# Kernel tuning notes

Measured on AMD Instinct MI355X. Metric: run time of the kernel, lower is better.

## Reference

```python
import jax, jax.numpy as jnp
import numpy as np

N_NODES = 100_000
N_EDGES_RAND = 800_000
N_GRAPHS = 2048
IN_FEATS = 74        # CanonicalAtomFeaturizer size
HEADS = 4            # dgllife GAT default num_heads
OUT_FEATS = 32       # dgllife GAT default hidden_feats=[32,32]
PRED_DIM = 128
NEG_SLOPE = 0.2      # dgllife default alpha


def setup_inputs() -> dict:
    key = jax.random.key(0)
    ks = jax.random.split(key, 16)
    feats = jax.random.normal(ks[0], (N_NODES, IN_FEATS), jnp.float32)
    src_r = jax.random.randint(ks[1], (N_EDGES_RAND,), 0, N_NODES, dtype=jnp.int32)
    dst_r = jax.random.randint(ks[2], (N_EDGES_RAND,), 0, N_NODES, dtype=jnp.int32)
    loops = jnp.arange(N_NODES, dtype=jnp.int32)  # self-loops -> no zero in-degree
    src = jnp.concatenate([src_r, loops])
    dst = jnp.concatenate([dst_r, loops])
    # sorted, every graph non-empty, ~49 nodes per molecule
    graph_ids = ((jnp.arange(N_NODES, dtype=jnp.int64) * N_GRAPHS) // N_NODES).astype(jnp.int32)

    def lin(k, i, o):
        return (jax.random.normal(k, (i, o), jnp.float32) / np.sqrt(i)).astype(jnp.float32)

    HF = HEADS * OUT_FEATS
    return {
        'feats': feats, 'src': src, 'dst': dst, 'graph_ids': graph_ids,
        'fc1_w': lin(ks[3], IN_FEATS, HF),
        'attn_l1': jax.random.normal(ks[4], (HEADS, OUT_FEATS), jnp.float32) * 0.1,
        'attn_r1': jax.random.normal(ks[5], (HEADS, OUT_FEATS), jnp.float32) * 0.1,
        'res1_w': lin(ks[6], IN_FEATS, HF),   # residual proj (in != heads*out)
        'bias1': jnp.zeros((HF,), jnp.float32),
        'fc2_w': lin(ks[7], HF, HF),
        'attn_l2': jax.random.normal(ks[8], (HEADS, OUT_FEATS), jnp.float32) * 0.1,
        'attn_r2': jax.random.normal(ks[9], (HEADS, OUT_FEATS), jnp.float32) * 0.1,
        'bias2': jnp.zeros((HF,), jnp.float32),
        'ww': lin(ks[10], OUT_FEATS, 1),
        'wb': jnp.zeros((1,), jnp.float32),
        'tw': lin(ks[11], 2 * OUT_FEATS, PRED_DIM),
        'tb': jnp.zeros((PRED_DIM,), jnp.float32),
    }


def _gat_conv(h, src, dst, fc_w, attn_l, attn_r, bias, res):
    # h: (N, Din) -> (N, H, F). Faithful to dgl.nn.GATConv (bias=True, residual=True).
    N = h.shape[0]
    feat = (h @ fc_w).reshape(N, HEADS, OUT_FEATS)          # (N,H,F)
    el = jnp.sum(feat * attn_l, axis=-1)                    # (N,H)
    er = jnp.sum(feat * attn_r, axis=-1)                    # (N,H)
    e = jax.nn.leaky_relu(el[src] + er[dst], NEG_SLOPE)     # (E,H)
    # edge softmax over incoming edges of each dst node (numerically stable)
    emax = jax.ops.segment_max(e, dst, num_segments=N)      # (N,H)
    ee = jnp.exp(e - emax[dst])
    denom = jax.ops.segment_sum(ee, dst, num_segments=N)    # (N,H)
    a = ee / denom[dst]                                     # (E,H)
    rst = jax.ops.segment_sum(a[:, :, None] * feat[src], dst, num_segments=N)  # (N,H,F)
    return rst + res + bias.reshape(1, HEADS, OUT_FEATS)


def reference(feats, src, dst, graph_ids, fc1_w, attn_l1, attn_r1, res1_w, bias1,
              fc2_w, attn_l2, attn_r2, bias2, ww, wb, tw, tb):
    N = feats.shape[0]
    # Layer 1: residual needs projection (74 != 128); agg 'flatten' + ELU
    res1 = (feats @ res1_w).reshape(N, HEADS, OUT_FEATS)
    h1 = _gat_conv(feats, src, dst, fc1_w, attn_l1, attn_r1, bias1, res1)
    h1 = jax.nn.elu(h1.reshape(N, HEADS * OUT_FEATS))
    # Layer 2: identity residual (128 == heads*out); agg 'mean', no activation
    res2 = h1.reshape(N, HEADS, OUT_FEATS)
    h2 = _gat_conv(h1, src, dst, fc2_w, attn_l2, attn_r2, bias2, res2)
    node_feats = jnp.mean(h2, axis=1)                       # (N, 32)
    # WeightedSumAndMax readout
    w = jax.nn.sigmoid(node_feats @ ww + wb)                # (N,1)
    h_sum = jax.ops.segment_sum(w * node_feats, graph_ids, num_segments=N_GRAPHS)
    h_max = jax.ops.segment_max(node_feats, graph_ids, num_segments=N_GRAPHS)
    g = jnp.concatenate([h_sum, h_max], axis=-1)            # (B, 64)
    return g @ tw + tb                                      # (B, PRED_DIM)
```

## Files before the change

kernel.cpp:

```cpp
#include <hip/hip_runtime.h>
#include <hip/hip_bf16.h>


#define HEADS 4
#define OUTF 32
#define HF 128
#define IN_FEATS 74
#define PRED_DIM 128
#define NEG_SLOPE 0.2f
#define NEG_INF_ENC 0x007fffffu
#define LOG2E 1.4426950408889634f
#define KP1 48
#define KP2 64
#define LSTR1 52
#define LSTR2 68

typedef __hip_bfloat16 bf16;
typedef __hip_bfloat162 bf16x2;
typedef __attribute__((ext_vector_type(8))) short bf16x8v;
typedef __attribute__((ext_vector_type(4))) float f32x4v;
typedef __attribute__((ext_vector_type(2))) float f32x2v;

__device__ __forceinline__ unsigned enc_f(float f) {
  unsigned u = __float_as_uint(f);
  return (u & 0x80000000u) ? ~u : (u | 0x80000000u);
}
__device__ __forceinline__ float dec_f(unsigned k) {
  return (k & 0x80000000u) ? __uint_as_float(k & 0x7fffffffu)
                           : __uint_as_float(~k);
}
__device__ __forceinline__ unsigned pack_bf16(float a, float b) {
  bf16x2 h = __float22bfloat162_rn(make_float2(a, b));
  return *(unsigned*)&h;
}
__device__ __forceinline__ float2 unpack_bf16(unsigned u) {
  bf16x2 h = *(bf16x2*)&u;
  return __bfloat1622float2(h);
}
__device__ __forceinline__ float lrelu(float v) {
  return fmaxf(v, NEG_SLOPE * v);
}

__global__ __launch_bounds__(256) void hist_prep(
    const int* __restrict__ dst, int* __restrict__ deg,
    int* __restrict__ rank, float* __restrict__ hsum,
    unsigned* __restrict__ hmax, int E, int g32,
    const float* __restrict__ W1, const float* __restrict__ W2,
    const float* __restrict__ W3, unsigned* __restrict__ WT1,
    unsigned* __restrict__ WT2, unsigned* __restrict__ WT3) {
  int t = blockIdx.x * 256 + threadIdx.x;
  if (t < g32) {
    hsum[t] = 0.f;
    hmax[t] = NEG_INF_ENC;
  }
  if (t < 128 * KP1) {
    int c = t / KP1, kp = t % KP1;
    int k = kp * 2;
    float a1 = (k < IN_FEATS) ? W1[k * HF + c] : 0.f;
    float b1 = (k + 1 < IN_FEATS) ? W1[(k + 1) * HF + c] : 0.f;
    float a2 = (k < IN_FEATS) ? W2[k * HF + c] : 0.f;
    float b2 = (k + 1 < IN_FEATS) ? W2[(k + 1) * HF + c] : 0.f;
    WT1[t] = pack_bf16(a1, b1);
    WT2[t] = pack_bf16(a2, b2);
  } else if (t - 128 * KP1 < 128 * KP2) {
    int u = t - 128 * KP1;
    int c = u / KP2, kp = u % KP2;
    int k = kp * 2;
    WT3[u] = pack_bf16(W3[k * HF + c], W3[(k + 1) * HF + c]);
  }
  if (t < E) rank[t] = atomicAdd(&deg[dst[t]], 1);
}

__global__ __launch_bounds__(256) void scan12_kernel(
    const int* __restrict__ deg, int* __restrict__ row_ptr,
    int* __restrict__ bsum, int* __restrict__ bpre,
    int* __restrict__ ticket, int N, int E) {
  const int base = blockIdx.x * 2048;
  const int tbase = base + threadIdx.x * 8;
  int vals[8];
  int tsum = 0;
#pragma unroll
  for (int i = 0; i < 8; ++i) {
    int idx = tbase + i;
    vals[i] = (idx < N) ? deg[idx] : 0;
    tsum += vals[i];
  }
  const int lane = threadIdx.x & 63, wv = threadIdx.x >> 6;
  int incl = tsum;
#pragma unroll
  for (int off = 1; off < 64; off <<= 1) {
    int nv = __shfl_up(incl, off);
    if (lane >= off) incl += nv;
  }
  __shared__ int wsum[4];
  __shared__ int isLast;
  if (lane == 63) wsum[wv] = incl;
  __syncthreads();
  int woff = 0;
  for (int w = 0; w < wv; ++w) woff += wsum[w];
  int run = woff + incl - tsum;
#pragma unroll
  for (int i = 0; i < 8; ++i) {
    int idx = tbase + i;
    if (idx < N) row_ptr[idx] = run;
    run += vals[i];
  }
  if (threadIdx.x == 255) {
    bsum[blockIdx.x] = woff + incl;
    __threadfence();
    int t = atomicAdd(ticket, 1);
    isLast = (t == (int)gridDim.x - 1);
  }
  __syncthreads();
  if (isLast) {
    if (threadIdx.x < 64) {
      __threadfence();
      const int NB = gridDim.x;
      int running = 0;
      for (int c = 0; c < NB; c += 64) {
        int v = (c + lane < NB) ? bsum[c + lane] : 0;
        int incl2 = v;
#pragma unroll
        for (int off = 1; off < 64; off <<= 1) {
          int nv = __shfl_up(incl2, off);
          if (lane >= off) incl2 += nv;
        }
        if (c + lane < NB) bpre[c + lane] = running + incl2 - v;
        running += __shfl(incl2, 63);
      }
    }
    __syncthreads();
    if (threadIdx.x == 0) row_ptr[N] = E - bpre[N >> 11];
  }
}


template <int K>
__device__ __forceinline__ bf16x8v load_a_f32(const float* __restrict__ X,
                                              int row, int N, int ks, int q) {
  unsigned v[4] = {0u, 0u, 0u, 0u};
  if (row < N) {
    const float* base = X + (size_t)row * K;
    int k = ks * 32 + q * 8;
#pragma unroll
    for (int j = 0; j < 4; ++j) {
      int kk = k + j * 2;
      if (kk + 1 < K) {
        float2 f = *(const float2*)&base[kk];
        v[j] = pack_bf16(f.x, f.y);
      } else if (kk < K) {
        v[j] = pack_bf16(base[kk], 0.f);
      }
    }
  }
  union { unsigned u[4]; bf16x8v v8; } r;
  r.u[0] = v[0]; r.u[1] = v[1]; r.u[2] = v[2]; r.u[3] = v[3];
  return r.v8;
}

template <int KP, int LSTR, int THREADS>
__device__ __forceinline__ void stage_w(const unsigned* __restrict__ WT,
                                        unsigned* wl, int tid) {
#pragma unroll
  for (int u = tid; u < 128 * (KP / 4); u += THREADS) {
    int row = u / (KP / 4), c4 = u % (KP / 4);
    uint4 v = *(const uint4*)&WT[row * KP + c4 * 4];
    *(uint4*)&wl[row * LSTR + c4 * 4] = v;
  }
}

__device__ __forceinline__ void scores_epilogue_sw(
    const f32x4v* acc, const float* __restrict__ attn_l,
    const float* __restrict__ attn_r, float* __restrict__ el,
    float* __restrict__ er, int node, int q, int lane, int N) {
  float pl[4], pr[4];
#pragma unroll
  for (int h = 0; h < 4; ++h) {
    float sl = 0.f, sr = 0.f;
#pragma unroll
    for (int r = 0; r < 4; ++r) {
      float c0 = acc[2 * h][r], c1 = acc[2 * h + 1][r];
      sl = fmaf(c0, attn_l[h * 32 + q * 4 + r], sl);
      sl = fmaf(c1, attn_l[h * 32 + 16 + q * 4 + r], sl);
      sr = fmaf(c0, attn_r[h * 32 + q * 4 + r], sr);
      sr = fmaf(c1, attn_r[h * 32 + 16 + q * 4 + r], sr);
    }
    sl += __shfl_xor(sl, 16);
    sl += __shfl_xor(sl, 32);
    sr += __shfl_xor(sr, 16);
    sr += __shfl_xor(sr, 32);
    pl[h] = sl * LOG2E;
    pr[h] = sr * LOG2E;
  }
  if (lane < 16 && node < N) {
    *(float4*)&el[(size_t)node * 4] = make_float4(pl[0], pl[1], pl[2], pl[3]);
    *(float4*)&er[(size_t)node * 4] = make_float4(pr[0], pr[1], pr[2], pr[3]);
  }
}

__device__ __forceinline__ void store_ct(const f32x4v* acc,
                                         bf16* __restrict__ out, int node,
                                         int q, int N) {
  if (node < N) {
#pragma unroll
    for (int t = 0; t < 8; ++t) {
      unsigned lo = pack_bf16(acc[t][0], acc[t][1]);
      unsigned hi = pack_bf16(acc[t][2], acc[t][3]);
      *(uint2*)&out[(size_t)node * HF + t * 16 + q * 4] = make_uint2(lo, hi);
    }
  }
}

__global__ __launch_bounds__(512) void scat_mfma1(
    const int* __restrict__ src, const int* __restrict__ dst,
    const int* __restrict__ row_ptr, const int* __restrict__ bpre,
    const int* __restrict__ rank, int* __restrict__ ssorted, int E, int gblk,
    const float* __restrict__ X, const unsigned* __restrict__ WT1,
    const unsigned* __restrict__ WT2, const float* __restrict__ attn_l,
    const float* __restrict__ attn_r, bf16* __restrict__ outA,
    bf16* __restrict__ outB, float* __restrict__ el, float* __restrict__ er,
    int N) {
  __shared__ __align__(16) unsigned wlds[2][128 * LSTR1];
  if ((int)blockIdx.x >= gblk) {
    int e = ((int)blockIdx.x - gblk) * 512 + threadIdx.x;
    if (e >= E) return;
    if (e < 16) ssorted[E + e] = 0;
    int d = dst[e];
    ssorted[row_ptr[d] + bpre[d >> 11] + rank[e]] = src[e];
    return;
  }
  const int tid = threadIdx.x;
  stage_w<KP1, LSTR1, 512>(WT1, &wlds[0][0], tid);
  stage_w<KP1, LSTR1, 512>(WT2, &wlds[1][0], tid);
  __syncthreads();

  const int w = tid >> 6;
  const int lane = tid & 63;
  const int cc = lane & 15;
  const int q = lane >> 4;
  const int n0 = blockIdx.x * 128;
  const int node = n0 + w * 16 + cc;

  f32x4v acc1[8], acc2[8];
#pragma unroll
  for (int t = 0; t < 8; ++t) {
    acc1[t] = f32x4v{0.f, 0.f, 0.f, 0.f};
    acc2[t] = f32x4v{0.f, 0.f, 0.f, 0.f};
  }

  constexpr int KSTEPS = (IN_FEATS + 31) / 32;
#pragma unroll
  for (int ks = 0; ks < KSTEPS; ++ks) {
    bf16x8v a = load_a_f32<IN_FEATS>(X, node, N, ks, q);
#pragma unroll
    for (int t = 0; t < 8; ++t) {
      bf16x8v b1 =
          *(const bf16x8v*)&wlds[0][(t * 16 + cc) * LSTR1 + ks * 16 + q * 4];
      bf16x8v b2 =
          *(const bf16x8v*)&wlds[1][(t * 16 + cc) * LSTR1 + ks * 16 + q * 4];
      acc1[t] = __builtin_amdgcn_mfma_f32_16x16x32_bf16(b1, a, acc1[t], 0, 0, 0);
      acc2[t] = __builtin_amdgcn_mfma_f32_16x16x32_bf16(b2, a, acc2[t], 0, 0, 0);
    }
  }
  store_ct(acc1, outA, node, q, N);
  store_ct(acc2, outB, node, q, N);
  scores_epilogue_sw(acc1, attn_l, attn_r, el, er, node, q, lane, N);
}

template <int K, int KP, int LSTR>
__global__ __launch_bounds__(512) void mfma_gemm(
    const bf16* __restrict__ X, const unsigned* __restrict__ WT,
    const float* __restrict__ attn_l, const float* __restrict__ attn_r,
    bf16* __restrict__ out, float* __restrict__ el, float* __restrict__ er,
    int N) {
  __shared__ __align__(16) unsigned wlds[128 * LSTR];
  const int tid = threadIdx.x;
  stage_w<KP, LSTR, 512>(WT, wlds, tid);
  __syncthreads();

  const int w = tid >> 6;
  const int lane = tid & 63;
  const int cc = lane & 15;
  const int q = lane >> 4;
  const int n0 = blockIdx.x * 128;
  const int node = n0 + w * 16 + cc;

  f32x4v acc[8];
#pragma unroll
  for (int t = 0; t < 8; ++t) acc[t] = f32x4v{0.f, 0.f, 0.f, 0.f};

  constexpr int KSTEPS = (K + 31) / 32;
#pragma unroll
  for (int ks = 0; ks < KSTEPS; ++ks) {
    bf16x8v a = *(const bf16x8v*)&X[(size_t)node * K + ks * 32 + q * 8];
#pragma unroll
    for (int t = 0; t < 8; ++t) {
      bf16x8v b =
          *(const bf16x8v*)&wlds[(t * 16 + cc) * LSTR + ks * 16 + q * 4];
      acc[t] = __builtin_amdgcn_mfma_f32_16x16x32_bf16(b, a, acc[t], 0, 0, 0);
    }
  }
  store_ct(acc, out, node, q, N);
  scores_epilogue_sw(acc, attn_l, attn_r, el, er, node, q, lane, N);
}


#define E8_LOAD(i, e_)                                                      \
  const int s##i = __builtin_amdgcn_readfirstlane(ssorted[e_]);             \
  const float xl##i = el[(unsigned)s##i * HEADS + h];                       \
  const unsigned fu##i = *(const unsigned*)&feat[(unsigned)s##i * HF + c2];
#define E8_CALC(i)                                                          \
  {                                                                         \
    float xx = __builtin_amdgcn_exp2f(lrelu(xl##i + ern));                  \
    f32x2v ff;                                                              \
    ff.x = __uint_as_float(fu##i << 16);                                    \
    ff.y = __uint_as_float(fu##i & 0xffff0000u);                            \
    ssum += xx;                                                             \
    axy = __builtin_elementwise_fma(f32x2v{xx, xx}, ff, axy);               \
  }
#define E8_CALC_PRED(i, e_)                                                 \
  {                                                                         \
    float xx = __builtin_amdgcn_exp2f(lrelu(xl##i + ern));                  \
    xx = ((e_) + i < re) ? xx : 0.f;                                        \
    f32x2v ff;                                                              \
    ff.x = __uint_as_float(fu##i << 16);                                    \
    ff.y = __uint_as_float(fu##i & 0xffff0000u);                            \
    ssum += xx;                                                             \
    axy = __builtin_elementwise_fma(f32x2v{xx, xx}, ff, axy);               \
  }

#define AGG_LOOP                                                            \
  f32x2v axy = {0.f, 0.f};                                                  \
  float ssum = 0.f;                                                         \
  const int dg = re - rb;                                                   \
  if (dg <= 8) {                                                            \
    E8_LOAD(0, rb) E8_LOAD(1, rb + 1) E8_LOAD(2, rb + 2)                    \
    E8_LOAD(3, rb + 3) E8_LOAD(4, rb + 4) E8_LOAD(5, rb + 5)                \
    E8_LOAD(6, rb + 6) E8_LOAD(7, rb + 7)                                   \
    E8_CALC_PRED(0, rb) E8_CALC_PRED(1, rb) E8_CALC_PRED(2, rb)             \
    E8_CALC_PRED(3, rb) E8_CALC_PRED(4, rb) E8_CALC_PRED(5, rb)             \
    E8_CALC_PRED(6, rb) E8_CALC_PRED(7, rb)                                 \
  } else if (dg <= 16) {                                                    \
    E8_LOAD(0, rb) E8_LOAD(1, rb + 1) E8_LOAD(2, rb + 2)                    \
    E8_LOAD(3, rb + 3) E8_LOAD(4, rb + 4) E8_LOAD(5, rb + 5)                \
    E8_LOAD(6, rb + 6) E8_LOAD(7, rb + 7)                                   \
    E8_LOAD(8, rb + 8) E8_LOAD(9, rb + 9) E8_LOAD(10, rb + 10)              \
    E8_LOAD(11, rb + 11) E8_LOAD(12, rb + 12) E8_LOAD(13, rb + 13)          \
    E8_LOAD(14, rb + 14) E8_LOAD(15, rb + 15)                               \
    E8_CALC(0) E8_CALC(1) E8_CALC(2) E8_CALC(3)                             \
    E8_CALC(4) E8_CALC(5) E8_CALC(6) E8_CALC(7)                             \
    E8_CALC_PRED(8, rb) E8_CALC_PRED(9, rb) E8_CALC_PRED(10, rb)            \
    E8_CALC_PRED(11, rb) E8_CALC_PRED(12, rb) E8_CALC_PRED(13, rb)          \
    E8_CALC_PRED(14, rb) E8_CALC_PRED(15, rb)                               \
  } else {                                                                  \
    int e = rb;                                                             \
    for (; e + 8 <= re; e += 8) {                                           \
      E8_LOAD(0, e) E8_LOAD(1, e + 1) E8_LOAD(2, e + 2) E8_LOAD(3, e + 3)   \
      E8_LOAD(4, e + 4) E8_LOAD(5, e + 5) E8_LOAD(6, e + 6)                 \
      E8_LOAD(7, e + 7)                                                     \
      E8_CALC(0) E8_CALC(1) E8_CALC(2) E8_CALC(3)                           \
      E8_CALC(4) E8_CALC(5) E8_CALC(6) E8_CALC(7)                           \
    }                                                                       \
    if (e < re) {                                                           \
      E8_LOAD(0, e) E8_LOAD(1, e + 1) E8_LOAD(2, e + 2) E8_LOAD(3, e + 3)   \
      E8_LOAD(4, e + 4) E8_LOAD(5, e + 5) E8_LOAD(6, e + 6)                 \
      E8_LOAD(7, e + 7)                                                     \
      E8_CALC_PRED(0, e) E8_CALC_PRED(1, e) E8_CALC_PRED(2, e)              \
      E8_CALC_PRED(3, e) E8_CALC_PRED(4, e) E8_CALC_PRED(5, e)              \
      E8_CALC_PRED(6, e) E8_CALC_PRED(7, e)                                 \
    }                                                                       \
  }                                                                         \
  float ax = axy.x, ay = axy.y;

__global__ __launch_bounds__(256) void agg1_fused(
    const int* __restrict__ row_ptr, const int* __restrict__ bpre,
    const int* __restrict__ ssorted, const float* __restrict__ el,
    const float* __restrict__ er, const bf16* __restrict__ feat,
    const bf16* __restrict__ res, bf16* __restrict__ H,
    const float* __restrict__ bias, int N) {
  int n = blockIdx.x * 4 + (threadIdx.x >> 6);
  if (n >= N) return;
  const int lane = threadIdx.x & 63;
  const int c2 = lane * 2, h = lane >> 4;
  const int rb =
      __builtin_amdgcn_readfirstlane(row_ptr[n] + bpre[n >> 11]);
  const int re =
      __builtin_amdgcn_readfirstlane(row_ptr[n + 1] + bpre[(n + 1) >> 11]);
  const float ern = er[(unsigned)n * HEADS + h];

  AGG_LOOP

  float inv = 1.f / ssum;
  float2 r = unpack_bf16(*(const unsigned*)&res[(unsigned)n * HF + c2]);
  float2 bi = *(const float2*)&bias[c2];
  float vx = fmaf(ax, inv, r.x + bi.x);
  float vy = fmaf(ay, inv, r.y + bi.y);
  vx = (vx > 0.f) ? vx : expm1f(vx);
  vy = (vy > 0.f) ? vy : expm1f(vy);
  *(unsigned*)&H[(unsigned)n * HF + c2] = pack_bf16(vx, vy);
}

__global__ __launch_bounds__(256) void agg2_fused(
    const int* __restrict__ row_ptr, const int* __restrict__ bpre,
    const int* __restrict__ ssorted, const float* __restrict__ el,
    const float* __restrict__ er, const bf16* __restrict__ feat,
    const bf16* __restrict__ h1, const float* __restrict__ bias,
    const float* __restrict__ ww, const float* __restrict__ wb,
    const int* __restrict__ gids, float* __restrict__ hsum,
    unsigned* __restrict__ hmax, int N) {
  int n = blockIdx.x * 4 + (threadIdx.x >> 6);
  if (n >= N) return;
  const int lane = threadIdx.x & 63;
  const int c2 = lane * 2, h = lane >> 4;
  const int rb =
      __builtin_amdgcn_readfirstlane(row_ptr[n] + bpre[n >> 11]);
  const int re =
      __builtin_amdgcn_readfirstlane(row_ptr[n + 1] + bpre[(n + 1) >> 11]);
  const float ern = er[(unsigned)n * HEADS + h];

  AGG_LOOP

  float inv = 1.f / ssum;
  float2 r = unpack_bf16(*(const unsigned*)&h1[(unsigned)n * HF + c2]);
  float2 bi = *(const float2*)&bias[c2];
  ax = fmaf(ax, inv, r.x + bi.x);
  ay = fmaf(ay, inv, r.y + bi.y);
#pragma unroll
  for (int off = 16; off < 64; off <<= 1) {
    ax += __shfl_xor(ax, off);
    ay += __shfl_xor(ay, off);
  }
  ax *= 0.25f;
  ay *= 0.25f;
  int c = c2 & 31;
  float d = fmaf(ax, ww[c], ay * ww[c + 1]);
#pragma unroll
  for (int off = 1; off < 16; off <<= 1) d += __shfl_xor(d, off);
  float wv = 1.f / (1.f + __expf(-(d + wb[0])));
  if (lane < 16) {
    int g = gids[n];
    atomicAdd(&hsum[g * OUTF + c], wv * ax);
    atomicAdd(&hsum[g * OUTF + c + 1], wv * ay);
    atomicMax(&hmax[g * OUTF + c], enc_f(ax));
    atomicMax(&hmax[g * OUTF + c + 1], enc_f(ay));
  }
}

__global__ __launch_bounds__(256) void final_gemm_kernel(
    const float* __restrict__ hsum, const unsigned* __restrict__ hmax,
    const float* __restrict__ tw, const float* __restrict__ tb,
    float* __restrict__ out, int G) {
  __shared__ float tws[64 * PRED_DIM];
  for (int i = threadIdx.x; i < 64 * PRED_DIM; i += 256) tws[i] = tw[i];
  __syncthreads();
  int g = blockIdx.x * 2 + (threadIdx.x >> 7);
  int p = threadIdx.x & 127;
  if (g >= G) return;
  float acc = tb[p];
#pragma unroll
  for (int k = 0; k < OUTF; ++k)
    acc = fmaf(hsum[g * OUTF + k], tws[k * PRED_DIM + p], acc);
#pragma unroll
  for (int k = 0; k < OUTF; ++k)
    acc = fmaf(dec_f(hmax[g * OUTF + k]), tws[(OUTF + k) * PRED_DIM + p], acc);
  out[(size_t)g * PRED_DIM + p] = acc;
}

static inline int cdiv(long long a, int b) { return (int)((a + b - 1) / b); }

extern "C" void kernel_launch(void* const* d_in, const int* in_sizes, int n_in,
                              void* d_out, int out_size, void* d_ws,
                              size_t ws_size, hipStream_t stream) {
  const float* feats   = (const float*)d_in[0];
  const int*   src     = (const int*)d_in[1];
  const int*   dst     = (const int*)d_in[2];
  const int*   gids    = (const int*)d_in[3];
  const float* fc1_w   = (const float*)d_in[4];
  const float* attn_l1 = (const float*)d_in[5];
  const float* attn_r1 = (const float*)d_in[6];
  const float* res1_w  = (const float*)d_in[7];
  const float* bias1   = (const float*)d_in[8];
  const float* fc2_w   = (const float*)d_in[9];
  const float* attn_l2 = (const float*)d_in[10];
  const float* attn_r2 = (const float*)d_in[11];
  const float* bias2   = (const float*)d_in[12];
  const float* ww      = (const float*)d_in[13];
  const float* wb      = (const float*)d_in[14];
  const float* tw      = (const float*)d_in[15];
  const float* tb      = (const float*)d_in[16];
  float* out = (float*)d_out;

  const int N = in_sizes[0] / IN_FEATS;
  const int E = in_sizes[1];
  const int G = out_size / PRED_DIM;
  const int NB = cdiv(N, 2048);

  bf16* A = (bf16*)d_ws;
  bf16* B = A + (size_t)N * HF;
  bf16* H = B + (size_t)N * HF;
  float* el = (float*)(H + (size_t)N * HF);
  float* er = el + (size_t)N * HEADS;
  float* hsum = er + (size_t)N * HEADS;
  unsigned* hmax = (unsigned*)(hsum + (size_t)G * OUTF);
  int* deg     = (int*)(hmax + (size_t)G * OUTF);
  int* ticket  = deg + N;
  int* row_ptr = deg + N + 1;
  int* ssorted = row_ptr + (N + 1);
  int* rank    = ssorted + E + 16;
  int* bsum    = rank + E;
  int* bpre    = bsum + NB;
  unsigned* WT1 = (unsigned*)(((uintptr_t)(bpre + NB) + 15) &
                              ~(uintptr_t)15);
  unsigned* WT2 = WT1 + 128 * KP1;
  unsigned* WT3 = WT2 + 128 * KP1;

  const int gblk = cdiv(N, 128);
  const int nwblk = cdiv(N, 4);
  const int SB = cdiv(E, 256);
  const int SB512 = cdiv(E, 512);

  hipMemsetAsync(deg, 0, (size_t)(N + 1) * sizeof(int), stream);
  hist_prep<<<SB, 256, 0, stream>>>(dst, deg, rank, hsum, hmax, E, G * OUTF,
                                    fc1_w, res1_w, fc2_w, WT1, WT2, WT3);
  scan12_kernel<<<NB, 256, 0, stream>>>(deg, row_ptr, bsum, bpre, ticket, N,
                                        E);

  scat_mfma1<<<gblk + SB512, 512, 0, stream>>>(
      src, dst, row_ptr, bpre, rank, ssorted, E, gblk, feats, WT1, WT2,
      attn_l1, attn_r1, A, B, el, er, N);
  agg1_fused<<<nwblk, 256, 0, stream>>>(row_ptr, bpre, ssorted, el, er, A, B,
                                        H, bias1, N);

  mfma_gemm<HF, KP2, LSTR2><<<gblk, 512, 0, stream>>>(
      H, WT3, attn_l2, attn_r2, A, el, er, N);
  agg2_fused<<<nwblk, 256, 0, stream>>>(row_ptr, bpre, ssorted, el, er, A, H,
                                        bias2, ww, wb, gids, hsum, hmax, N);

  final_gemm_kernel<<<cdiv(G, 2), 256, 0, stream>>>(hsum, hmax, tw, tb, out, G);
}
```

Measured before the change: 315.0 us.

## Overlap second-half layer-1 aggregation with first-half layer-2 GEMM in one launch

```diff
diff --git a/kernel.cpp b/kernel.cpp
--- a/kernel.cpp
+++ b/kernel.cpp
@@ -209,6 +209,35 @@
       *(uint2*)&out[(size_t)node * HF + t * 16 + q * 4] = make_uint2(lo, hi);
     }
   }
+}
+
+__device__ __forceinline__ void gemm2_body(
+    const bf16* __restrict__ X, const unsigned* wlds,
+    const float* __restrict__ attn_l, const float* __restrict__ attn_r,
+    bf16* __restrict__ out, float* __restrict__ el2,
+    float* __restrict__ er2, int n0, int tid, int N) {
+  const int lane = tid & 63;
+  const int cc = lane & 15;
+  const int q = lane >> 4;
+  const int w = tid >> 6;
+  const int node = n0 + w * 16 + cc;
+
+  f32x4v acc[8];
+#pragma unroll
+  for (int t = 0; t < 8; ++t) acc[t] = f32x4v{0.f, 0.f, 0.f, 0.f};
+
+#pragma unroll
+  for (int ks = 0; ks < 4; ++ks) {
+    bf16x8v a = *(const bf16x8v*)&X[(size_t)node * HF + ks * 32 + q * 8];
+#pragma unroll
+    for (int t = 0; t < 8; ++t) {
+      bf16x8v b =
+          *(const bf16x8v*)&wlds[(t * 16 + cc) * LSTR2 + ks * 16 + q * 4];
+      acc[t] = __builtin_amdgcn_mfma_f32_16x16x32_bf16(b, a, acc[t], 0, 0, 0);
+    }
+  }
+  store_ct(acc, out, node, q, N);
+  scores_epilogue_sw(acc, attn_l, attn_r, el2, er2, node, q, lane, N);
 }
 
 __global__ __launch_bounds__(512) void scat_mfma1(
@@ -267,43 +296,17 @@
   scores_epilogue_sw(acc1, attn_l, attn_r, el, er, node, q, lane, N);
 }
 
-template <int K, int KP, int LSTR>
-__global__ __launch_bounds__(512) void mfma_gemm(
+__global__ __launch_bounds__(512) void mfma_gemm2(
     const bf16* __restrict__ X, const unsigned* __restrict__ WT,
     const float* __restrict__ attn_l, const float* __restrict__ attn_r,
-    bf16* __restrict__ out, float* __restrict__ el, float* __restrict__ er,
-    int N) {
-  __shared__ __align__(16) unsigned wlds[128 * LSTR];
-  const int tid = threadIdx.x;
-  stage_w<KP, LSTR, 512>(WT, wlds, tid);
+    bf16* __restrict__ out, float* __restrict__ el2, float* __restrict__ er2,
+    int t0, int N) {
+  __shared__ __align__(16) unsigned wlds[128 * LSTR2];
+  stage_w<KP2, LSTR2, 512>(WT, wlds, threadIdx.x);
   __syncthreads();
-
-  const int w = tid >> 6;
-  const int lane = tid & 63;
-  const int cc = lane & 15;
-  const int q = lane >> 4;
-  const int n0 = blockIdx.x * 128;
-  const int node = n0 + w * 16 + cc;
-
-  f32x4v acc[8];
-#pragma unroll
-  for (int t = 0; t < 8; ++t) acc[t] = f32x4v{0.f, 0.f, 0.f, 0.f};
-
-  constexpr int KSTEPS = (K + 31) / 32;
-#pragma unroll
-  for (int ks = 0; ks < KSTEPS; ++ks) {
-    bf16x8v a = *(const bf16x8v*)&X[(size_t)node * K + ks * 32 + q * 8];
-#pragma unroll
-    for (int t = 0; t < 8; ++t) {
-      bf16x8v b =
-          *(const bf16x8v*)&wlds[(t * 16 + cc) * LSTR + ks * 16 + q * 4];
-      acc[t] = __builtin_amdgcn_mfma_f32_16x16x32_bf16(b, a, acc[t], 0, 0, 0);
-    }
-  }
-  store_ct(acc, out, node, q, N);
-  scores_epilogue_sw(acc, attn_l, attn_r, el, er, node, q, lane, N);
-}
-
+  gemm2_body(X, wlds, attn_l, attn_r, out, el2, er2,
+             (t0 + (int)blockIdx.x) * 128, threadIdx.x, N);
+}
 
 #define E8_LOAD(i, e_)                                                      \
   const int s##i = __builtin_amdgcn_readfirstlane(ssorted[e_]);             \
@@ -372,15 +375,12 @@
   }                                                                         \
   float ax = axy.x, ay = axy.y;
 
-__global__ __launch_bounds__(256) void agg1_fused(
-    const int* __restrict__ row_ptr, const int* __restrict__ bpre,
-    const int* __restrict__ ssorted, const float* __restrict__ el,
-    const float* __restrict__ er, const bf16* __restrict__ feat,
-    const bf16* __restrict__ res, bf16* __restrict__ H,
-    const float* __restrict__ bias, int N) {
-  int n = blockIdx.x * 4 + (threadIdx.x >> 6);
-  if (n >= N) return;
-  const int lane = threadIdx.x & 63;
+__device__ __forceinline__ void agg1_body(
+    int n, int lane, const int* __restrict__ row_ptr,
+    const int* __restrict__ bpre, const int* __restrict__ ssorted,
+    const float* __restrict__ el, const float* __restrict__ er,
+    const bf16* __restrict__ feat, const bf16* __restrict__ res,
+    bf16* __restrict__ H, const float* __restrict__ bias) {
   const int c2 = lane * 2, h = lane >> 4;
   const int rb =
       __builtin_amdgcn_readfirstlane(row_ptr[n] + bpre[n >> 11]);
@@ -398,6 +398,41 @@
   vx = (vx > 0.f) ? vx : expm1f(vx);
   vy = (vy > 0.f) ? vy : expm1f(vy);
   *(unsigned*)&H[(unsigned)n * HF + c2] = pack_bf16(vx, vy);
+}
+
+__global__ __launch_bounds__(256) void agg1_fused(
+    const int* __restrict__ row_ptr, const int* __restrict__ bpre,
+    const int* __restrict__ ssorted, const float* __restrict__ el,
+    const float* __restrict__ er, const bf16* __restrict__ feat,
+    const bf16* __restrict__ res, bf16* __restrict__ H,
+    const float* __restrict__ bias, int nlimit) {
+  int n = blockIdx.x * 4 + (threadIdx.x >> 6);
+  if (n >= nlimit) return;
+  agg1_body(n, threadIdx.x & 63, row_ptr, bpre, ssorted, el, er, feat, res,
+            H, bias);
+}
+
+__global__ __launch_bounds__(512) void agg1_mfma2(
+    const int* __restrict__ row_ptr, const int* __restrict__ bpre,
+    const int* __restrict__ ssorted, const float* __restrict__ el,
+    const float* __restrict__ er, const bf16* __restrict__ feat,
+    const bf16* __restrict__ res, bf16* __restrict__ H,
+    const float* __restrict__ bias, int Nh, int N, int aggblk,
+    const unsigned* __restrict__ WT, const float* __restrict__ attn_l2,
+    const float* __restrict__ attn_r2, bf16* __restrict__ out2,
+    float* __restrict__ el2, float* __restrict__ er2) {
+  __shared__ __align__(16) unsigned wlds[128 * LSTR2];
+  if ((int)blockIdx.x < aggblk) {
+    int n = Nh + blockIdx.x * 8 + (threadIdx.x >> 6);
+    if (n >= N) return;
+    agg1_body(n, threadIdx.x & 63, row_ptr, bpre, ssorted, el, er, feat, res,
+              H, bias);
+    return;
+  }
+  stage_w<KP2, LSTR2, 512>(WT, wlds, threadIdx.x);
+  __syncthreads();
+  gemm2_body(H, wlds, attn_l2, attn_r2, out2, el2, er2,
+             ((int)blockIdx.x - aggblk) * 128, threadIdx.x, N);
 }
 
 __global__ __launch_bounds__(256) void agg2_fused(
@@ -498,9 +533,12 @@
   bf16* A = (bf16*)d_ws;
   bf16* B = A + (size_t)N * HF;
   bf16* H = B + (size_t)N * HF;
-  float* el = (float*)(H + (size_t)N * HF);
+  bf16* C = H + (size_t)N * HF;
+  float* el = (float*)(C + (size_t)N * HF);
   float* er = el + (size_t)N * HEADS;
-  float* hsum = er + (size_t)N * HEADS;
+  float* el2 = er + (size_t)N * HEADS;
+  float* er2 = el2 + (size_t)N * HEADS;
+  float* hsum = er2 + (size_t)N * HEADS;
   unsigned* hmax = (unsigned*)(hsum + (size_t)G * OUTF);
   int* deg     = (int*)(hmax + (size_t)G * OUTF);
   int* ticket  = deg + N;
@@ -515,26 +553,33 @@
   unsigned* WT3 = WT2 + 128 * KP1;
 
   const int gblk = cdiv(N, 128);
-  const int nwblk = cdiv(N, 4);
-  const int SB = cdiv(E, 256);
+  const int g2a = gblk / 2;
+  const int Nh = g2a * 128;
+  const int aggblk = cdiv(N - Nh, 8);
   const int SB512 = cdiv(E, 512);
 
   hipMemsetAsync(deg, 0, (size_t)(N + 1) * sizeof(int), stream);
-  hist_prep<<<SB, 256, 0, stream>>>(dst, deg, rank, hsum, hmax, E, G * OUTF,
-                                    fc1_w, res1_w, fc2_w, WT1, WT2, WT3);
+  hist_prep<<<cdiv(E, 256), 256, 0, stream>>>(
+      dst, deg, rank, hsum, hmax, E, G * OUTF, fc1_w, res1_w, fc2_w, WT1,
+      WT2, WT3);
   scan12_kernel<<<NB, 256, 0, stream>>>(deg, row_ptr, bsum, bpre, ticket, N,
                                         E);
 
   scat_mfma1<<<gblk + SB512, 512, 0, stream>>>(
       src, dst, row_ptr, bpre, rank, ssorted, E, gblk, feats, WT1, WT2,
       attn_l1, attn_r1, A, B, el, er, N);
-  agg1_fused<<<nwblk, 256, 0, stream>>>(row_ptr, bpre, ssorted, el, er, A, B,
-                                        H, bias1, N);
-
-  mfma_gemm<HF, KP2, LSTR2><<<gblk, 512, 0, stream>>>(
-      H, WT3, attn_l2, attn_r2, A, el, er, N);
-  agg2_fused<<<nwblk, 256, 0, stream>>>(row_ptr, bpre, ssorted, el, er, A, H,
-                                        bias2, ww, wb, gids, hsum, hmax, N);
+
+  agg1_fused<<<cdiv(Nh, 4), 256, 0, stream>>>(row_ptr, bpre, ssorted, el, er,
+                                              A, B, H, bias1, Nh);
+  agg1_mfma2<<<aggblk + g2a, 512, 0, stream>>>(
+      row_ptr, bpre, ssorted, el, er, A, B, H, bias1, Nh, N, aggblk, WT3,
+      attn_l2, attn_r2, C, el2, er2);
+  mfma_gemm2<<<gblk - g2a, 512, 0, stream>>>(H, WT3, attn_l2, attn_r2, C,
+                                             el2, er2, g2a, N);
+
+  agg2_fused<<<cdiv(N, 4), 256, 0, stream>>>(row_ptr, bpre, ssorted, el2,
+                                             er2, C, H, bias2, ww, wb, gids,
+                                             hsum, hmax, N);
 
   final_gemm_kernel<<<cdiv(G, 2), 256, 0, stream>>>(hsum, hmax, tw, tb, out, G);
 }
```

Result: slower. 326.4 us (+3.6%).
